# Performance work log

Hardware: AMD Instinct MI355X
Metric: run time of the kernel (lower is better)

The kernel has to match this reference:

```python
import jax, jax.numpy as jnp
import numpy as np

N = 2048          # num atoms
ATOM_D = 64       # atom embedding dim
H = 8             # num heads
NB = 8            # num bond types
D = ATOM_D * H    # 512, Q/K/V output dim
NEG_SLOPE = 0.2


def setup_inputs() -> dict:
    key = jax.random.key(0)
    ks = jax.random.split(key, 12)
    inp = {
        "atom_embeddings": jax.random.normal(ks[0], (N, ATOM_D), dtype=jnp.float32),
        # bond type per (i, j); -1 means no bond (masked)
        "edges": jax.random.randint(ks[1], (N, N), -1, NB, dtype=jnp.int32),
        "Qw": jax.random.normal(ks[2], (ATOM_D, D), dtype=jnp.float32) / np.sqrt(ATOM_D),
        "Qb": jnp.zeros((D,), dtype=jnp.float32),
        "Kw": jax.random.normal(ks[3], (ATOM_D, D), dtype=jnp.float32) / np.sqrt(ATOM_D),
        "Kb": jnp.zeros((D,), dtype=jnp.float32),
        "Vw": jax.random.normal(ks[4], (ATOM_D, D), dtype=jnp.float32) / np.sqrt(ATOM_D),
        "Vb": jnp.zeros((D,), dtype=jnp.float32),
        # per-bond-type attention weights: (NB, 2*D, H), xavier-ish scale
        "a": jax.random.normal(ks[5], (NB, 2 * D, H), dtype=jnp.float32) * np.sqrt(2.0 / (2 * D + H)) * 1.414,
        "Pw": jax.random.normal(ks[6], (D, ATOM_D), dtype=jnp.float32) / np.sqrt(D),
        "Pb": jnp.zeros((ATOM_D,), dtype=jnp.float32),
    }
    return inp


def reference(atom_embeddings, edges, Qw, Qb, Kw, Kb, Vw, Vb, a, Pw, Pb):
    n, d = atom_embeddings.shape
    nb, two_d, h = a.shape
    D_ = two_d // 2
    Q = atom_embeddings @ Qw + Qb          # (N, D)
    K = atom_embeddings @ Kw + Kb          # (N, D)
    V = atom_embeddings @ Vw + Vb          # (N, D)

    # a[k] applies to concat(Q_i, K_j): split into src / dst halves
    A1 = a[:, :D_, :]                      # (NB, D, H)
    A2 = a[:, D_:, :]                      # (NB, D, H)
    # precompute per-node, per-bond-type partial scores (avoids the dense
    # one-hot scatter of the original: direct per-edge-type weight indexing)
    S1 = jnp.einsum('id,kdh->ikh', Q, A1)  # (N, NB, H)
    S2 = jnp.einsum('jd,kdh->jkh', K, A2)  # (N, NB, H)

    kidx = jnp.clip(edges, 0, nb - 1)      # (N, N)
    rows = jnp.arange(n)
    # e[i,j,h] = S1[i, edges[i,j], h] + S2[j, edges[i,j], h]
    e = S1[rows[:, None], kidx] + S2[rows[None, :], kidx]   # (N, N, H)
    valid = (edges >= 0)[..., None]
    # masked edges get all-zero rows in the original scatter -> score exactly 0
    e = jnp.where(valid, jax.nn.leaky_relu(e, negative_slope=NEG_SLOPE), 0.0)

    attn = jax.nn.softmax(e, axis=1)       # softmax over neighbor j
    Vh = V.reshape(n, h, d)                # (N, H, atom_d)
    out = jnp.einsum('ijh,jhd->ihd', attn, Vh).reshape(n, h * d)
    return out @ Pw + Pb                   # (N, atom_d)
```

## Files before the change

kernel.cpp:

```cpp
#include <hip/hip_runtime.h>

#define NN 2048
#define AD 64
#define HH 8
#define DD 512
#define NEG 0.2f

typedef float f32x4 __attribute__((ext_vector_type(4)));
typedef _Float16 half8 __attribute__((ext_vector_type(8)));
typedef _Float16 half2v __attribute__((ext_vector_type(2)));
typedef unsigned short u16;
typedef unsigned int u32;
typedef u16 u16x8 __attribute__((ext_vector_type(8)));

__global__ __launch_bounds__(256) void prep_kernel(
    const float* __restrict__ Qw, const float* __restrict__ Qb,
    const float* __restrict__ Kw, const float* __restrict__ Kb,
    const float* __restrict__ A,
    float* __restrict__ W1, float* __restrict__ W2, float* __restrict__ c12) {
  __shared__ float As[512][8];
  __shared__ float Ws8[8][516];
  __shared__ float red[4][8][8];
  __shared__ float red2[8][8];
  int t = threadIdx.x;
  int b = blockIdx.x;
  int mat = b >> 6;
  int k = (b >> 3) & 7;
  int dg = b & 7;
  int d0 = dg * 8;
  const float* Asrc = A + (size_t)k * 8192 + mat * 4096;
  const float* Wsrc = (mat ? Kw : Qw) + (size_t)d0 * DD;

  float* Asf = &As[0][0];
  for (int idx = t; idx < 4096; idx += 256) Asf[idx] = Asrc[idx];
  for (int idx = t; idx < 4096; idx += 256) {
    int dd = idx >> 9, c = idx & 511;
    Ws8[dd][c] = Wsrc[idx];
  }
  __syncthreads();

  int dd = t & 7, h = (t >> 3) & 7, cs = t >> 6;
  int cbase = cs * 128;
  float acc = 0.f;
#pragma unroll 4
  for (int c = 0; c < 128; ++c) {
    acc += Ws8[dd][cbase + c] * As[cbase + c][h];
  }
  red[cs][dd][h] = acc;
  __syncthreads();
  if (t < 64) {
    int dd2 = t >> 3, h2 = t & 7;
    float v = red[0][dd2][h2] + red[1][dd2][h2] + red[2][dd2][h2] + red[3][dd2][h2];
    (mat ? W2 : W1)[(d0 + dd2) * 64 + k * 8 + h2] = v;
  }
  if (dg == 0) {
    if (t < 64) {
      int h2 = t >> 3, seg = t & 7;
      const float* bs = mat ? Kb : Qb;
      float a2 = 0.f;
      for (int i = 0; i < 64; ++i) {
        int c = seg * 64 + i;
        a2 += bs[c] * As[c][h2];
      }
      red2[h2][seg] = a2;
    }
    __syncthreads();
    if (t < 8) {
      float s = 0.f;
#pragma unroll
      for (int seg = 0; seg < 8; ++seg) s += red2[t][seg];
      c12[mat * 64 + k * 8 + t] = s;
    }
  }
}

__global__ __launch_bounds__(256) void stab_kernel(
    const float* __restrict__ X,
    const float* __restrict__ W1, const float* __restrict__ W2,
    const float* __restrict__ c12,
    u16* __restrict__ TS1, u16* __restrict__ TS2) {
  __shared__ float W1L[64][65];
  __shared__ float W2L[64][65];
  __shared__ float XS[16][65];
  __shared__ __align__(16) u16 T1S[16][128];
  __shared__ __align__(16) u16 T2S[16][128];
  int t = threadIdx.x;
  int r0 = blockIdx.x * 16;
  for (int i = t; i < 4096; i += 256) {
    int d = i >> 6, kh = i & 63;
    W1L[d][kh] = W1[i];
    W2L[d][kh] = W2[i];
  }
  {
    int r = t >> 4, c = (t & 15) * 4;
    float4 xv = *(const float4*)&X[(size_t)(r0 + r) * AD + c];
    XS[r][c] = xv.x; XS[r][c + 1] = xv.y; XS[r][c + 2] = xv.z; XS[r][c + 3] = xv.w;
  }
  __syncthreads();
  int r = t >> 4, khq = t & 15;
  float a1[4], a2[4];
#pragma unroll
  for (int i = 0; i < 4; ++i) {
    a1[i] = c12[khq * 4 + i];
    a2[i] = c12[64 + khq * 4 + i];
  }
  for (int d = 0; d < 64; ++d) {
    float x = XS[r][d];
#pragma unroll
    for (int i = 0; i < 4; ++i) {
      a1[i] += x * W1L[d][khq * 4 + i];
      a2[i] += x * W2L[d][khq * 4 + i];
    }
  }
#pragma unroll
  for (int i = 0; i < 4; ++i) {
    int kh = khq * 4 + i, k = kh >> 3, h = kh & 7;
    int kki = (k ^ (r & 7)) << 4;
    _Float16 p1 = (_Float16)(__expf(a1[i]) * 0.25f);
    _Float16 n1 = (_Float16)(__expf(NEG * a1[i]) * 0.25f);
    _Float16 p2 = (_Float16)(__expf(a2[i]) * 0.25f);
    _Float16 n2 = (_Float16)(__expf(NEG * a2[i]) * 0.25f);
    T1S[r][kki + h]     = __builtin_bit_cast(u16, p1);
    T1S[r][kki + 8 + h] = __builtin_bit_cast(u16, n1);
    T2S[r][kki + h]     = __builtin_bit_cast(u16, p2);
    T2S[r][kki + 8 + h] = __builtin_bit_cast(u16, n2);
  }
  __syncthreads();
  {
    const u16* s1 = &T1S[0][0];
    const u16* s2 = &T2S[0][0];
    *(u16x8*)&TS1[(size_t)r0 * 128 + t * 8] = *(const u16x8*)&s1[t * 8];
    *(u16x8*)&TS2[(size_t)r0 * 128 + t * 8] = *(const u16x8*)&s2[t * 8];
  }
}

__global__ __launch_bounds__(256) void vth_kernel(
    const float* __restrict__ X,
    const float* __restrict__ Vw, const float* __restrict__ Vb,
    u16* __restrict__ VtH) {
  __shared__ float Xs[64][68];
  int t = threadIdx.x;
  int tile = blockIdx.x;
  int r0 = (tile >> 2) * 64;
  int d0 = (tile & 3) * 128;

  for (int idx = t; idx < 64 * 64; idx += 256) {
    int r = idx >> 6, c = idx & 63;
    Xs[r][c] = X[(size_t)(r0 + r) * AD + c];
  }
  __syncthreads();

  int tr = t >> 5;
  int td = t & 31;
  int d = d0 + td * 4;
  float4 bias = *(const float4*)&Vb[d];
  float4 acc[8];
#pragma unroll
  for (int i = 0; i < 8; ++i) acc[i] = bias;
  for (int c = 0; c < 64; ++c) {
    float4 w = *(const float4*)&Vw[c * DD + d];
#pragma unroll
    for (int i = 0; i < 8; ++i) {
      float x = Xs[tr * 8 + i][c];
      acc[i].x += x * w.x; acc[i].y += x * w.y;
      acc[i].z += x * w.z; acc[i].w += x * w.w;
    }
  }
#pragma unroll
  for (int c = 0; c < 4; ++c) {
    u16x8 o;
#pragma unroll
    for (int i = 0; i < 8; ++i) {
      float fv = (c == 0) ? acc[i].x : (c == 1) ? acc[i].y
               : (c == 2) ? acc[i].z : acc[i].w;
      _Float16 hf = (_Float16)fv;
      o[i] = __builtin_bit_cast(u16, hf);
    }
    *(u16x8*)&VtH[(size_t)(d + c) * NN + r0 + tr * 8] = o;
  }
}

__global__ __launch_bounds__(512, 4) void attn_mfma_kernel(
    const int* __restrict__ E,
    const u16* __restrict__ TS1, const u16* __restrict__ TS2,
    const u16* __restrict__ VtH,
    float* __restrict__ PART, float* __restrict__ LPART) {
  __shared__ _Float16 s1t[16 * 128];
  __shared__ _Float16 s2t[2][64 * 128];
  __shared__ _Float16 PA[2][8][16][72];
  int t = threadIdx.x;
  int w = t >> 6, lane = t & 63;
  int li = lane & 15, q = lane >> 4;
  int m = lane & 31;
  int i_loc = w * 2 + (lane >> 5);
  int it = blockIdx.x >> 2, ch = blockIdx.x & 3;
  int i0 = it * 16, jch = ch * 512;

  const half8 SIX8 = {(_Float16)0.0625f, (_Float16)0.0625f, (_Float16)0.0625f,
                      (_Float16)0.0625f, (_Float16)0.0625f, (_Float16)0.0625f,
                      (_Float16)0.0625f, (_Float16)0.0625f};
  const half8 ONE8 = {(_Float16)1.0f, (_Float16)1.0f, (_Float16)1.0f,
                      (_Float16)1.0f, (_Float16)1.0f, (_Float16)1.0f,
                      (_Float16)1.0f, (_Float16)1.0f};

  if (t < 256) {
    *(u16x8*)&s1t[t * 8] = *(const u16x8*)&TS1[(size_t)i0 * 128 + t * 8];
  }
  {
    const u16* src = TS2 + (size_t)jch * 128;
    *(u16x8*)&s2t[0][t * 8]        = *(const u16x8*)&src[t * 8];
    *(u16x8*)&s2t[0][4096 + t * 8] = *(const u16x8*)&src[4096 + t * 8];
  }
  u16x8 stA = *(const u16x8*)&TS2[(size_t)(jch + 64) * 128 + t * 8];
  u16x8 stB = *(const u16x8*)&TS2[(size_t)(jch + 64) * 128 + 4096 + t * 8];
  const int* Erow = E + (size_t)(i0 + i_loc) * NN;
  int2 eCur = *(const int2*)(Erow + jch + 2 * m);
  int2 eNxt = *(const int2*)(Erow + jch + 64 + 2 * m);
  __syncthreads();

  f32x4 acc[4];
#pragma unroll
  for (int n = 0; n < 4; ++n) acc[n] = (f32x4){0.f, 0.f, 0.f, 0.f};
  f32x4 acc_l = (f32x4){0.f, 0.f, 0.f, 0.f};
  int cur = 0;

#pragma unroll 1
  for (int jt = 0; jt < 8; ++jt) {
    int jb = jch + jt * 64;

    u16x8 stA2, stB2;
    int2 eN2 = eNxt;
    if (jt < 6) {
      const u16* src = TS2 + (size_t)(jb + 128) * 128;
      stA2 = *(const u16x8*)&src[t * 8];
      stB2 = *(const u16x8*)&src[4096 + t * 8];
      eN2 = *(const int2*)(Erow + jb + 128 + 2 * m);
    }

    half8 bfrag[4][2];
#pragma unroll
    for (int n = 0; n < 4; ++n)
#pragma unroll
      for (int s = 0; s < 2; ++s) {
        const u16* p = &VtH[(size_t)(w * 64 + n * 16 + li) * NN + jb + s * 32 + q * 8];
        bfrag[n][s] = *(const half8*)p;
      }

    const _Float16* s1row = &s1t[i_loc * 128];
    const _Float16* s2row = &s2t[cur][0];
    half8 pmj[2];
#pragma unroll
    for (int jj = 0; jj < 2; ++jj) {
      int ev = jj ? eCur.y : eCur.x;
      int j = 2 * m + jj;
      int k = min(max(ev, 0), 7);
      int kki = (k ^ (i_loc & 7)) << 4;
      int kkj = (k ^ (j & 7)) << 4;
      half8 ip = *(const half8*)&s1row[kki];
      half8 in_ = *(const half8*)&s1row[kki + 8];
      half8 jp = *(const half8*)&s2row[j * 128 + kkj];
      half8 jn = *(const half8*)&s2row[j * 128 + kkj + 8];
      half8 pp = ip * jp;
      half8 pn = in_ * jn;
      half8 pm = __builtin_elementwise_max(pp, pn);
      if (ev < 0) pm = SIX8;
      pmj[jj] = pm;
    }
#pragma unroll
    for (int h = 0; h < 8; ++h) {
      half2v wv = {pmj[0][h], pmj[1][h]};
      *(half2v*)&PA[cur][h][i_loc][2 * m] = wv;
    }

    if (jt < 7) {
      *(u16x8*)&s2t[cur ^ 1][t * 8]        = stA;
      *(u16x8*)&s2t[cur ^ 1][4096 + t * 8] = stB;
    }
    __syncthreads();

    half8 af0 = *(const half8*)&PA[cur][w][li][q * 8];
    half8 af1 = *(const half8*)&PA[cur][w][li][32 + q * 8];
    __builtin_amdgcn_s_setprio(1);
#pragma unroll
    for (int n = 0; n < 4; ++n) {
      acc[n] = __builtin_amdgcn_mfma_f32_16x16x32_f16(af0, bfrag[n][0], acc[n], 0, 0, 0);
      acc[n] = __builtin_amdgcn_mfma_f32_16x16x32_f16(af1, bfrag[n][1], acc[n], 0, 0, 0);
    }
    acc_l = __builtin_amdgcn_mfma_f32_16x16x32_f16(af0, ONE8, acc_l, 0, 0, 0);
    acc_l = __builtin_amdgcn_mfma_f32_16x16x32_f16(af1, ONE8, acc_l, 0, 0, 0);
    __builtin_amdgcn_s_setprio(0);

    stA = stA2; stB = stB2;
    eCur = eNxt; eNxt = eN2;
    cur ^= 1;
  }

  if (li == 0) {
#pragma unroll
    for (int r = 0; r < 4; ++r)
      LPART[((size_t)ch * NN + i0 + q * 4 + r) * 8 + w] = acc_l[r];
  }

  float* base = PART + (size_t)ch * NN * DD;
#pragma unroll
  for (int n = 0; n < 4; ++n) {
#pragma unroll
    for (int r = 0; r < 4; ++r) {
      int row = i0 + q * 4 + r;
      int col = w * 64 + n * 16 + li;
      base[(size_t)row * DD + col] = acc[n][r];
    }
  }
}

__global__ __launch_bounds__(256) void proj_kernel(
    const float* __restrict__ PART, const float* __restrict__ LPART,
    const float* __restrict__ Pw, const float* __restrict__ Pb,
    float* __restrict__ out) {
  __shared__ __align__(16) float preS[4][512];
  __shared__ float linv[4][8];
  int t = threadIdx.x;
  int r0 = blockIdx.x * 4;
  if (t < 32) {
    int i = t >> 3, h = t & 7;
    float s = 0.f;
#pragma unroll
    for (int c = 0; c < 4; ++c)
      s += LPART[(size_t)c * NN * 8 + (size_t)(r0 + i) * 8 + h];
    linv[i][h] = 1.0f / s;
  }
  __syncthreads();
  for (int idx = t; idx < 4 * 128; idx += 256) {
    int i = idx >> 7, hd = (idx & 127) * 4;
    float4 v = {0.f, 0.f, 0.f, 0.f};
#pragma unroll
    for (int c = 0; c < 4; ++c) {
      float4 p = *(const float4*)&PART[(size_t)c * NN * DD + (size_t)(r0 + i) * DD + hd];
      v.x += p.x; v.y += p.y; v.z += p.z; v.w += p.w;
    }
    float li2 = linv[i][hd >> 6];
    v.x *= li2; v.y *= li2; v.z *= li2; v.w *= li2;
    *(float4*)&preS[i][hd] = v;
  }
  __syncthreads();
  int c = t & 63, rq = t >> 6;
  float acc0 = Pb[c];
  for (int hq = 0; hq < 128; ++hq) {
    int hd = hq * 4;
    float4 p0 = *(const float4*)&preS[rq][hd];
    float w0 = Pw[(hd + 0) * 64 + c];
    float w1 = Pw[(hd + 1) * 64 + c];
    float w2 = Pw[(hd + 2) * 64 + c];
    float w3 = Pw[(hd + 3) * 64 + c];
    acc0 += p0.x * w0 + p0.y * w1 + p0.z * w2 + p0.w * w3;
  }
  out[(size_t)(r0 + rq) * 64 + c] = acc0;
}

extern "C" void kernel_launch(void* const* d_in, const int* in_sizes, int n_in,
                              void* d_out, int out_size, void* d_ws, size_t ws_size,
                              hipStream_t stream) {
  const float* X  = (const float*)d_in[0];
  const int*   E  = (const int*)d_in[1];
  const float* Qw = (const float*)d_in[2];
  const float* Qb = (const float*)d_in[3];
  const float* Kw = (const float*)d_in[4];
  const float* Kb = (const float*)d_in[5];
  const float* Vw = (const float*)d_in[6];
  const float* Vb = (const float*)d_in[7];
  const float* A  = (const float*)d_in[8];
  const float* Pw = (const float*)d_in[9];
  const float* Pb = (const float*)d_in[10];
  float* out = (float*)d_out;

  float* ws = (float*)d_ws;
  const size_t ND = (size_t)NN * DD;
  float* PART  = ws;
  u16*   TS1   = (u16*)(ws + 4 * ND);
  u16*   TS2   = TS1 + (size_t)NN * 128;
  u16*   VtH   = TS2 + (size_t)NN * 128;
  float* LPART = (float*)(VtH + (size_t)DD * NN);
  float* W1    = LPART + (size_t)4 * NN * 8;
  float* W2    = W1 + 4096;
  float* c12   = W2 + 4096;

  prep_kernel<<<128, 256, 0, stream>>>(Qw, Qb, Kw, Kb, A, W1, W2, c12);
  vth_kernel<<<128, 256, 0, stream>>>(X, Vw, Vb, VtH);
  stab_kernel<<<128, 256, 0, stream>>>(X, W1, W2, c12, TS1, TS2);
  attn_mfma_kernel<<<512, 512, 0, stream>>>(E, TS1, TS2, VtH, PART, LPART);
  proj_kernel<<<512, 256, 0, stream>>>(PART, LPART, Pw, Pb, out);
}
```

Measured before the change: 79.35 us.

## Merge prep and V-projection kernels; prefetch V fragments one tile ahead

Folds the independent prep and V-projection kernels into one launch with 256 blocks split by block index, removing one kernel launch. In the attention kernel, the V B-fragments are register double-buffered: fragments for the next j-tile load while the current tile computes. The loop is manually unrolled by two so the LDS buffer index is a compile-time constant. __syncthreads is replaced by an explicit lgkmcnt wait plus s_barrier and a sched_barrier. The prefetch doubles the B-fragment registers, which could raise register pressure under launch_bounds(512,4).

Result: slower. 96.57 us (+21.7%).

```diff
diff --git a/kernel.cpp b/kernel.cpp
--- a/kernel.cpp
+++ b/kernel.cpp
@@ -13,63 +13,108 @@
 typedef unsigned int u32;
 typedef u16 u16x8 __attribute__((ext_vector_type(8)));
 
-__global__ __launch_bounds__(256) void prep_kernel(
+__global__ __launch_bounds__(256) void prep_vth_kernel(
     const float* __restrict__ Qw, const float* __restrict__ Qb,
     const float* __restrict__ Kw, const float* __restrict__ Kb,
     const float* __restrict__ A,
-    float* __restrict__ W1, float* __restrict__ W2, float* __restrict__ c12) {
+    const float* __restrict__ X,
+    const float* __restrict__ Vw, const float* __restrict__ Vb,
+    float* __restrict__ W1, float* __restrict__ W2, float* __restrict__ c12,
+    u16* __restrict__ VtH) {
   __shared__ float As[512][8];
   __shared__ float Ws8[8][516];
   __shared__ float red[4][8][8];
   __shared__ float red2[8][8];
+  __shared__ float Xs[64][68];
   int t = threadIdx.x;
   int b = blockIdx.x;
-  int mat = b >> 6;
-  int k = (b >> 3) & 7;
-  int dg = b & 7;
-  int d0 = dg * 8;
-  const float* Asrc = A + (size_t)k * 8192 + mat * 4096;
-  const float* Wsrc = (mat ? Kw : Qw) + (size_t)d0 * DD;
-
-  float* Asf = &As[0][0];
-  for (int idx = t; idx < 4096; idx += 256) Asf[idx] = Asrc[idx];
-  for (int idx = t; idx < 4096; idx += 256) {
-    int dd = idx >> 9, c = idx & 511;
-    Ws8[dd][c] = Wsrc[idx];
-  }
-  __syncthreads();
-
-  int dd = t & 7, h = (t >> 3) & 7, cs = t >> 6;
-  int cbase = cs * 128;
-  float acc = 0.f;
+  if (b < 128) {
+    int mat = b >> 6;
+    int k = (b >> 3) & 7;
+    int dg = b & 7;
+    int d0 = dg * 8;
+    const float* Asrc = A + (size_t)k * 8192 + mat * 4096;
+    const float* Wsrc = (mat ? Kw : Qw) + (size_t)d0 * DD;
+
+    float* Asf = &As[0][0];
+    for (int idx = t; idx < 4096; idx += 256) Asf[idx] = Asrc[idx];
+    for (int idx = t; idx < 4096; idx += 256) {
+      int dd = idx >> 9, c = idx & 511;
+      Ws8[dd][c] = Wsrc[idx];
+    }
+    __syncthreads();
+
+    int dd = t & 7, h = (t >> 3) & 7, cs = t >> 6;
+    int cbase = cs * 128;
+    float acc = 0.f;
 #pragma unroll 4
-  for (int c = 0; c < 128; ++c) {
-    acc += Ws8[dd][cbase + c] * As[cbase + c][h];
-  }
-  red[cs][dd][h] = acc;
-  __syncthreads();
-  if (t < 64) {
-    int dd2 = t >> 3, h2 = t & 7;
-    float v = red[0][dd2][h2] + red[1][dd2][h2] + red[2][dd2][h2] + red[3][dd2][h2];
-    (mat ? W2 : W1)[(d0 + dd2) * 64 + k * 8 + h2] = v;
-  }
-  if (dg == 0) {
+    for (int c = 0; c < 128; ++c) {
+      acc += Ws8[dd][cbase + c] * As[cbase + c][h];
+    }
+    red[cs][dd][h] = acc;
+    __syncthreads();
     if (t < 64) {
-      int h2 = t >> 3, seg = t & 7;
-      const float* bs = mat ? Kb : Qb;
-      float a2 = 0.f;
-      for (int i = 0; i < 64; ++i) {
-        int c = seg * 64 + i;
-        a2 += bs[c] * As[c][h2];
+      int dd2 = t >> 3, h2 = t & 7;
+      float v = red[0][dd2][h2] + red[1][dd2][h2] + red[2][dd2][h2] + red[3][dd2][h2];
+      (mat ? W2 : W1)[(d0 + dd2) * 64 + k * 8 + h2] = v;
+    }
+    if (dg == 0) {
+      if (t < 64) {
+        int h2 = t >> 3, seg = t & 7;
+        const float* bs = mat ? Kb : Qb;
+        float a2 = 0.f;
+        for (int i = 0; i < 64; ++i) {
+          int c = seg * 64 + i;
+          a2 += bs[c] * As[c][h2];
+        }
+        red2[h2][seg] = a2;
       }
-      red2[h2][seg] = a2;
+      __syncthreads();
+      if (t < 8) {
+        float s = 0.f;
+#pragma unroll
+        for (int seg = 0; seg < 8; ++seg) s += red2[t][seg];
+        c12[mat * 64 + k * 8 + t] = s;
+      }
+    }
+  } else {
+    int tile = b - 128;
+    int r0 = (tile >> 2) * 64;
+    int d0 = (tile & 3) * 128;
+
+    for (int idx = t; idx < 64 * 64; idx += 256) {
+      int r = idx >> 6, c = idx & 63;
+      Xs[r][c] = X[(size_t)(r0 + r) * AD + c];
     }
     __syncthreads();
-    if (t < 8) {
-      float s = 0.f;
-#pragma unroll
-      for (int seg = 0; seg < 8; ++seg) s += red2[t][seg];
-      c12[mat * 64 + k * 8 + t] = s;
+
+    int tr = t >> 5;
+    int td = t & 31;
+    int d = d0 + td * 4;
+    float4 bias = *(const float4*)&Vb[d];
+    float4 acc[8];
+#pragma unroll
+    for (int i = 0; i < 8; ++i) acc[i] = bias;
+    for (int c = 0; c < 64; ++c) {
+      float4 w = *(const float4*)&Vw[c * DD + d];
+#pragma unroll
+      for (int i = 0; i < 8; ++i) {
+        float x = Xs[tr * 8 + i][c];
+        acc[i].x += x * w.x; acc[i].y += x * w.y;
+        acc[i].z += x * w.z; acc[i].w += x * w.w;
+      }
+    }
+#pragma unroll
+    for (int c = 0; c < 4; ++c) {
+      u16x8 o;
+#pragma unroll
+      for (int i = 0; i < 8; ++i) {
+        float fv = (c == 0) ? acc[i].x : (c == 1) ? acc[i].y
+                 : (c == 2) ? acc[i].z : acc[i].w;
+        _Float16 hf = (_Float16)fv;
+        o[i] = __builtin_bit_cast(u16, hf);
+      }
+      *(u16x8*)&VtH[(size_t)(d + c) * NN + r0 + tr * 8] = o;
     }
   }
 }
@@ -134,52 +179,6 @@
   }
 }
 
-__global__ __launch_bounds__(256) void vth_kernel(
-    const float* __restrict__ X,
-    const float* __restrict__ Vw, const float* __restrict__ Vb,
-    u16* __restrict__ VtH) {
-  __shared__ float Xs[64][68];
-  int t = threadIdx.x;
-  int tile = blockIdx.x;
-  int r0 = (tile >> 2) * 64;
-  int d0 = (tile & 3) * 128;
-
-  for (int idx = t; idx < 64 * 64; idx += 256) {
-    int r = idx >> 6, c = idx & 63;
-    Xs[r][c] = X[(size_t)(r0 + r) * AD + c];
-  }
-  __syncthreads();
-
-  int tr = t >> 5;
-  int td = t & 31;
-  int d = d0 + td * 4;
-  float4 bias = *(const float4*)&Vb[d];
-  float4 acc[8];
-#pragma unroll
-  for (int i = 0; i < 8; ++i) acc[i] = bias;
-  for (int c = 0; c < 64; ++c) {
-    float4 w = *(const float4*)&Vw[c * DD + d];
-#pragma unroll
-    for (int i = 0; i < 8; ++i) {
-      float x = Xs[tr * 8 + i][c];
-      acc[i].x += x * w.x; acc[i].y += x * w.y;
-      acc[i].z += x * w.z; acc[i].w += x * w.w;
-    }
-  }
-#pragma unroll
-  for (int c = 0; c < 4; ++c) {
-    u16x8 o;
-#pragma unroll
-    for (int i = 0; i < 8; ++i) {
-      float fv = (c == 0) ? acc[i].x : (c == 1) ? acc[i].y
-               : (c == 2) ? acc[i].z : acc[i].w;
-      _Float16 hf = (_Float16)fv;
-      o[i] = __builtin_bit_cast(u16, hf);
-    }
-    *(u16x8*)&VtH[(size_t)(d + c) * NN + r0 + tr * 8] = o;
-  }
-}
-
 __global__ __launch_bounds__(512, 4) void attn_mfma_kernel(
     const int* __restrict__ E,
     const u16* __restrict__ TS1, const u16* __restrict__ TS2,
@@ -216,84 +215,98 @@
   const int* Erow = E + (size_t)(i0 + i_loc) * NN;
   int2 eCur = *(const int2*)(Erow + jch + 2 * m);
   int2 eNxt = *(const int2*)(Erow + jch + 64 + 2 * m);
+  half8 bf0[4][2], bf1[4][2];
+#pragma unroll
+  for (int n = 0; n < 4; ++n)
+#pragma unroll
+    for (int s = 0; s < 2; ++s)
+      bf0[n][s] = *(const half8*)&VtH[(size_t)(w * 64 + n * 16 + li) * NN +
+                                      jch + s * 32 + q * 8];
   __syncthreads();
 
   f32x4 acc[4];
 #pragma unroll
   for (int n = 0; n < 4; ++n) acc[n] = (f32x4){0.f, 0.f, 0.f, 0.f};
   f32x4 acc_l = (f32x4){0.f, 0.f, 0.f, 0.f};
-  int cur = 0;
+
+#define TILE_BODY(CUR, BFC, BFN, JT)                                          \
+  do {                                                                        \
+    int jb = jch + (JT) * 64;                                                 \
+                                     \
+    u16x8 stA2 = stA, stB2 = stB;                                             \
+    int2 eN2 = eNxt;                                                          \
+    if ((JT) < 6) {                                                           \
+      const u16* src = TS2 + (size_t)(jb + 128) * 128;                        \
+      stA2 = *(const u16x8*)&src[t * 8];                                      \
+      stB2 = *(const u16x8*)&src[4096 + t * 8];                               \
+      eN2 = *(const int2*)(Erow + jb + 128 + 2 * m);                          \
+    }                                                                         \
+                   \
+    {                                                                         \
+      int jbn = jch + (((JT) < 7) ? (JT) + 1 : 7) * 64;                       \
+      _Pragma("unroll")                                                       \
+      for (int n = 0; n < 4; ++n)                                             \
+        _Pragma("unroll")                                                     \
+        for (int s = 0; s < 2; ++s)                                           \
+          BFN[n][s] = *(const half8*)&VtH[(size_t)(w * 64 + n * 16 + li) * NN \
+                                          + jbn + s * 32 + q * 8];            \
+    }                                                                         \
+                                                      \
+    const _Float16* s1row = &s1t[i_loc * 128];                                \
+    const _Float16* s2row = &s2t[CUR][0];                                     \
+    half8 pmj[2];                                                             \
+    _Pragma("unroll")                                                         \
+    for (int jj = 0; jj < 2; ++jj) {                                          \
+      int ev = jj ? eCur.y : eCur.x;                                          \
+      int j = 2 * m + jj;                                                     \
+      int k = min(max(ev, 0), 7);                                             \
+      int kki = (k ^ (i_loc & 7)) << 4;                                       \
+      int kkj = (k ^ (j & 7)) << 4;                                           \
+      half8 ip = *(const half8*)&s1row[kki];                                  \
+      half8 in_ = *(const half8*)&s1row[kki + 8];                             \
+      half8 jp = *(const half8*)&s2row[j * 128 + kkj];                        \
+      half8 jn = *(const half8*)&s2row[j * 128 + kkj + 8];                    \
+      half8 pp = ip * jp;                                                     \
+      half8 pn = in_ * jn;                                                    \
+      half8 pm = __builtin_elementwise_max(pp, pn);                           \
+      if (ev < 0) pm = SIX8;                                                  \
+      pmj[jj] = pm;                                                           \
+    }                                                                         \
+    _Pragma("unroll")                                                         \
+    for (int h = 0; h < 8; ++h) {                                             \
+      half2v wv = {pmj[0][h], pmj[1][h]};                                     \
+      *(half2v*)&PA[CUR][h][i_loc][2 * m] = wv;                               \
+    }                                                                         \
+            \
+    if ((JT) < 7) {                                                           \
+      *(u16x8*)&s2t[(CUR) ^ 1][t * 8]        = stA;                           \
+      *(u16x8*)&s2t[(CUR) ^ 1][4096 + t * 8] = stB;                           \
+    }                                                                         \
+            \
+    asm volatile("s_waitcnt lgkmcnt(0)" ::: "memory");                        \
+    __builtin_amdgcn_s_barrier();                                             \
+    __builtin_amdgcn_sched_barrier(0);                                        \
+    half8 af0 = *(const half8*)&PA[CUR][w][li][q * 8];                        \
+    half8 af1 = *(const half8*)&PA[CUR][w][li][32 + q * 8];                   \
+    __builtin_amdgcn_s_setprio(1);                                            \
+    _Pragma("unroll")                                                         \
+    for (int n = 0; n < 4; ++n) {                                             \
+      acc[n] = __builtin_amdgcn_mfma_f32_16x16x32_f16(af0, BFC[n][0], acc[n], 0, 0, 0); \
+      acc[n] = __builtin_amdgcn_mfma_f32_16x16x32_f16(af1, BFC[n][1], acc[n], 0, 0, 0); \
+    }                                                                         \
+    acc_l = __builtin_amdgcn_mfma_f32_16x16x32_f16(af0, ONE8, acc_l, 0, 0, 0);\
+    acc_l = __builtin_amdgcn_mfma_f32_16x16x32_f16(af1, ONE8, acc_l, 0, 0, 0);\
+    __builtin_amdgcn_s_setprio(0);                                            \
+    stA = stA2; stB = stB2;                                                   \
+    eCur = eNxt; eNxt = eN2;                                                  \
+  } while (0)
 
 #pragma unroll 1
-  for (int jt = 0; jt < 8; ++jt) {
-    int jb = jch + jt * 64;
-
-    u16x8 stA2, stB2;
-    int2 eN2 = eNxt;
-    if (jt < 6) {
-      const u16* src = TS2 + (size_t)(jb + 128) * 128;
-      stA2 = *(const u16x8*)&src[t * 8];
-      stB2 = *(const u16x8*)&src[4096 + t * 8];
-      eN2 = *(const int2*)(Erow + jb + 128 + 2 * m);
-    }
-
-    half8 bfrag[4][2];
-#pragma unroll
-    for (int n = 0; n < 4; ++n)
-#pragma unroll
-      for (int s = 0; s < 2; ++s) {
-        const u16* p = &VtH[(size_t)(w * 64 + n * 16 + li) * NN + jb + s * 32 + q * 8];
-        bfrag[n][s] = *(const half8*)p;
-      }
-
-    const _Float16* s1row = &s1t[i_loc * 128];
-    const _Float16* s2row = &s2t[cur][0];
-    half8 pmj[2];
-#pragma unroll
-    for (int jj = 0; jj < 2; ++jj) {
-      int ev = jj ? eCur.y : eCur.x;
-      int j = 2 * m + jj;
-      int k = min(max(ev, 0), 7);
-      int kki = (k ^ (i_loc & 7)) << 4;
-      int kkj = (k ^ (j & 7)) << 4;
-      half8 ip = *(const half8*)&s1row[kki];
-      half8 in_ = *(const half8*)&s1row[kki + 8];
-      half8 jp = *(const half8*)&s2row[j * 128 + kkj];
-      half8 jn = *(const half8*)&s2row[j * 128 + kkj + 8];
-      half8 pp = ip * jp;
-      half8 pn = in_ * jn;
-      half8 pm = __builtin_elementwise_max(pp, pn);
-      if (ev < 0) pm = SIX8;
-      pmj[jj] = pm;
-    }
-#pragma unroll
-    for (int h = 0; h < 8; ++h) {
-      half2v wv = {pmj[0][h], pmj[1][h]};
-      *(half2v*)&PA[cur][h][i_loc][2 * m] = wv;
-    }
-
-    if (jt < 7) {
-      *(u16x8*)&s2t[cur ^ 1][t * 8]        = stA;
-      *(u16x8*)&s2t[cur ^ 1][4096 + t * 8] = stB;
-    }
-    __syncthreads();
-
-    half8 af0 = *(const half8*)&PA[cur][w][li][q * 8];
-    half8 af1 = *(const half8*)&PA[cur][w][li][32 + q * 8];
-    __builtin_amdgcn_s_setprio(1);
-#pragma unroll
-    for (int n = 0; n < 4; ++n) {
-      acc[n] = __builtin_amdgcn_mfma_f32_16x16x32_f16(af0, bfrag[n][0], acc[n], 0, 0, 0);
-      acc[n] = __builtin_amdgcn_mfma_f32_16x16x32_f16(af1, bfrag[n][1], acc[n], 0, 0, 0);
-    }
-    acc_l = __builtin_amdgcn_mfma_f32_16x16x32_f16(af0, ONE8, acc_l, 0, 0, 0);
-    acc_l = __builtin_amdgcn_mfma_f32_16x16x32_f16(af1, ONE8, acc_l, 0, 0, 0);
-    __builtin_amdgcn_s_setprio(0);
-
-    stA = stA2; stB = stB2;
-    eCur = eNxt; eNxt = eN2;
-    cur ^= 1;
-  }
+  for (int jt2 = 0; jt2 < 4; ++jt2) {
+    TILE_BODY(0, bf0, bf1, 2 * jt2);
+    TILE_BODY(1, bf1, bf0, 2 * jt2 + 1);
+  }
+#undef TILE_BODY
 
   if (li == 0) {
 #pragma unroll
@@ -384,8 +397,8 @@
   float* W2    = W1 + 4096;
   float* c12   = W2 + 4096;
 
-  prep_kernel<<<128, 256, 0, stream>>>(Qw, Qb, Kw, Kb, A, W1, W2, c12);
-  vth_kernel<<<128, 256, 0, stream>>>(X, Vw, Vb, VtH);
+  prep_vth_kernel<<<256, 256, 0, stream>>>(Qw, Qb, Kw, Kb, A, X, Vw, Vb,
+                                           W1, W2, c12, VtH);
   stab_kernel<<<128, 256, 0, stream>>>(X, W1, W2, c12, TS1, TS2);
   attn_mfma_kernel<<<512, 512, 0, stream>>>(E, TS1, TS2, VtH, PART, LPART);
   proj_kernel<<<512, 256, 0, stream>>>(PART, LPART, Pw, Pb, out);
```
